# Kernel tuning notes

Measured on AMD Instinct MI355X. Metric: run time of the kernel, lower is better.

Reference implementation:

```python
import jax, jax.numpy as jnp
import numpy as np
import math

D_MODEL = 1024
NUM_HEADS = 16
D_K = D_MODEL // NUM_HEADS
MAX_LEN = 512
B, S = 16, 512


def setup_inputs() -> dict:
    key = jax.random.key(0)
    ks = jax.random.split(key, 12)
    init = lambda k, shape, s=0.02: jax.random.normal(k, shape, dtype=jnp.float32) * s
    return {
        "query": jax.random.normal(ks[0], (B, S, D_MODEL), dtype=jnp.float32),
        "key": jax.random.normal(ks[1], (B, S, D_MODEL), dtype=jnp.float32),
        "value": jax.random.normal(ks[2], (B, S, D_MODEL), dtype=jnp.float32),
        "wq_w": init(ks[3], (D_MODEL, D_MODEL)),
        "wq_b": jnp.zeros((D_MODEL,), jnp.float32),
        "wk_w": init(ks[4], (D_MODEL, D_MODEL)),
        "wk_b": jnp.zeros((D_MODEL,), jnp.float32),
        "wv_w": init(ks[5], (D_MODEL, D_MODEL)),
        "wv_b": jnp.zeros((D_MODEL,), jnp.float32),
        "wo_w": init(ks[6], (D_MODEL, D_MODEL)),
        "wo_b": jnp.zeros((D_MODEL,), jnp.float32),
        "rel_bias": init(ks[7], (NUM_HEADS, MAX_LEN, MAX_LEN)),
    }


def reference(query, key, value, wq_w, wq_b, wk_w, wk_b, wv_w, wv_b, wo_w, wo_b, rel_bias):
    b, s, _ = query.shape
    scale = math.sqrt(D_K)
    # torch Linear: x @ W.T + b ; split heads -> [b, s, H, dk]
    Q = (query @ wq_w.T + wq_b).reshape(b, s, NUM_HEADS, D_K)
    K = (key @ wk_w.T + wk_b).reshape(b, s, NUM_HEADS, D_K)
    V = (value @ wv_w.T + wv_b).reshape(b, s, NUM_HEADS, D_K)
    # scores [b, H, s, t]
    scores = jnp.einsum("bshd,bthd->bhst", Q, K) / scale
    scores = scores + rel_bias[None, :, :s, :s]
    causal = jnp.triu(jnp.ones((s, s), dtype=bool), k=1)  # True above diagonal
    scores = jnp.where(causal[None, None, :, :], -jnp.inf, scores)
    attn = jax.nn.softmax(scores, axis=-1)  # dropout p=0 (eval)
    ctx = jnp.einsum("bhst,bthd->bshd", attn, V).reshape(b, s, D_MODEL)
    out = ctx @ wo_w.T + wo_b
    return out, attn.mean(axis=1)
```

## Files before the change

kernel.cpp:

```cpp
#include <hip/hip_runtime.h>
#include <hip/hip_bf16.h>
#include <math.h>

#define D_MODEL 1024
#define NUM_HEADS 16
#define D_K 64
#define BATCH 16
#define SEQ 512

typedef __attribute__((ext_vector_type(8))) short short8;
typedef __attribute__((ext_vector_type(4))) float floatx4;

__device__ inline unsigned short f2bf(float f) {
  __hip_bfloat16 h = __float2bfloat16(f);
  return *reinterpret_cast<unsigned short*>(&h);
}
__device__ inline float bf2f(unsigned short us) {
  unsigned u = ((unsigned)us) << 16;
  return __uint_as_float(u);
}

typedef const __attribute__((address_space(1))) unsigned int glb_u32;
typedef __attribute__((address_space(3))) unsigned int lds_u32;

__device__ inline void load16_to_lds(const void* g, void* l) {
  __builtin_amdgcn_global_load_lds((glb_u32*)(uintptr_t)g,
                                   (lds_u32*)(unsigned int)(uintptr_t)l, 16, 0,
                                   0);
}

__global__ __launch_bounds__(256) void conv_all(
    const float* __restrict__ q, const float* __restrict__ k,
    const float* __restrict__ v, const float* __restrict__ w0,
    const float* __restrict__ w1, const float* __restrict__ w2,
    const float* __restrict__ w3, unsigned short* __restrict__ xq,
    unsigned short* __restrict__ xk, unsigned short* __restrict__ xv,
    unsigned short* __restrict__ d0, unsigned short* __restrict__ d1,
    unsigned short* __restrict__ d2, unsigned short* __restrict__ d3) {
  const size_t MG = 1048576, WG = 131072;
  const size_t g = (size_t)blockIdx.x * 256 + threadIdx.x;
  const float* src;
  unsigned short* dst;
  size_t idx;
  if (g < 3 * MG) {
    const int r = (int)(g >> 20);
    idx = g & (MG - 1);
    src = (r == 0) ? q : (r == 1) ? k : v;
    dst = (r == 0) ? xq : (r == 1) ? xk : xv;
  } else {
    const size_t gw = g - 3 * MG;
    const int r = (int)(gw >> 17);
    idx = gw & (WG - 1);
    src = (r == 0) ? w0 : (r == 1) ? w1 : (r == 2) ? w2 : w3;
    dst = (r == 0) ? d0 : (r == 1) ? d1 : (r == 2) ? d2 : d3;
  }
  const float4 a = ((const float4*)src)[2 * idx];
  const float4 b = ((const float4*)src)[2 * idx + 1];
  short8 o;
  o[0] = f2bf(a.x); o[1] = f2bf(a.y); o[2] = f2bf(a.z); o[3] = f2bf(a.w);
  o[4] = f2bf(b.x); o[5] = f2bf(b.y); o[6] = f2bf(b.z); o[7] = f2bf(b.w);
  ((short8*)dst)[idx] = o;
}

__global__ __launch_bounds__(256) void qkv_gemm(
    const unsigned short* __restrict__ Xall,
    const unsigned short* __restrict__ Wall,
    const float* __restrict__ bq, const float* __restrict__ bk,
    const float* __restrict__ bv,
    unsigned short* __restrict__ QKout,
    unsigned short* __restrict__ Vt) {
  constexpr int K = 1024;
  const size_t ME = (size_t)BATCH * SEQ * D_MODEL;
  const size_t WE = (size_t)D_MODEL * D_MODEL;

  const int f = blockIdx.x + (blockIdx.y << 3) + (blockIdx.z << 9);
  const int virt = ((f & 7) * 192) + (f >> 3);
  const int xi = virt & 7;
  const int rest = virt >> 3;
  const int yi = rest & 63;
  const int z = rest >> 6;

  const unsigned short* A = Xall + (size_t)z * ME;
  const unsigned short* Bw = Wall + (size_t)z * WE;
  const float* bias = (z == 0) ? bq : (z == 1) ? bk : bv;

  __shared__ __align__(16) unsigned short sA[2][128 * 64];
  __shared__ __align__(16) unsigned short sB[2][128 * 64];
  const int tid = threadIdx.x;
  const int w = tid >> 6, lane = tid & 63;
  const int quad = lane >> 4, lq = lane & 15;
  const int wm = w >> 1, wn = w & 1;
  const int m0 = yi << 7, n0 = xi << 7;

  const int lrow8 = lane >> 3;
  const int sg = lane & 7;

  floatx4 acc[4][4];
#pragma unroll
  for (int i = 0; i < 4; ++i)
#pragma unroll
    for (int j = 0; j < 4; ++j) acc[i][j] = {0.f, 0.f, 0.f, 0.f};

  auto stage = [&](int buf, int kt) {
#pragma unroll
    for (int i = 0; i < 4; ++i) {
      const int row = (i << 5) + (w << 3) + lrow8;
      const int g = sg ^ (row & 7);
      const unsigned short* gA = A + (size_t)(m0 + row) * K + kt + (g << 3);
      const unsigned short* gB = Bw + (size_t)(n0 + row) * K + kt + (g << 3);
      load16_to_lds(gA, &sA[buf][((i << 5) + (w << 3)) * 64]);
      load16_to_lds(gB, &sB[buf][((i << 5) + (w << 3)) * 64]);
    }
  };

  stage(0, 0);
  __syncthreads();
  int cur = 0;
  for (int kt = 0; kt < K; kt += 64) {
    if (kt + 64 < K) stage(cur ^ 1, kt + 64);
#pragma unroll
    for (int s = 0; s < 2; ++s) {
      short8 aF[4], bF[4];
#pragma unroll
      for (int mi = 0; mi < 4; ++mi) {
        const int row = (wm << 6) + (mi << 4) + lq;
        const int g = ((s << 2) + quad) ^ (row & 7);
        aF[mi] = *(const short8*)&sA[cur][row * 64 + (g << 3)];
      }
#pragma unroll
      for (int ni = 0; ni < 4; ++ni) {
        const int row = (wn << 6) + (ni << 4) + lq;
        const int g = ((s << 2) + quad) ^ (row & 7);
        bF[ni] = *(const short8*)&sB[cur][row * 64 + (g << 3)];
      }
#pragma unroll
      for (int mi = 0; mi < 4; ++mi)
#pragma unroll
        for (int ni = 0; ni < 4; ++ni)
          acc[mi][ni] = __builtin_amdgcn_mfma_f32_16x16x32_bf16(
              aF[mi], bF[ni], acc[mi][ni], 0, 0, 0);
    }
    __syncthreads();
    cur ^= 1;
  }

#pragma unroll
  for (int ni = 0; ni < 4; ++ni) {
    const int n = n0 + (wn << 6) + (ni << 4) + lq;
    const float bn = bias[n];
    const int hh = n >> 6, dk = n & 63;
#pragma unroll
    for (int mi = 0; mi < 4; ++mi) {
      const int mb = m0 + (wm << 6) + (mi << 4) + (quad << 2);
      const int bb = mb >> 9, ss = mb & 511;
      if (z == 2) {
        ushort4 pk;
        pk.x = f2bf(acc[mi][ni][0] + bn);
        pk.y = f2bf(acc[mi][ni][1] + bn);
        pk.z = f2bf(acc[mi][ni][2] + bn);
        pk.w = f2bf(acc[mi][ni][3] + bn);
        *(ushort4*)&Vt[((size_t)(bb * NUM_HEADS + hh) * D_K + dk) * SEQ + ss] =
            pk;
      } else {
        unsigned short* dst = QKout + (size_t)z * ME;
#pragma unroll
        for (int r = 0; r < 4; ++r)
          dst[((size_t)(bb * NUM_HEADS + hh) * SEQ + ss + r) * D_K + dk] =
              f2bf(acc[mi][ni][r] + bn);
      }
    }
  }
}

__global__ __launch_bounds__(256) void out_gemm(
    const unsigned short* __restrict__ A, const unsigned short* __restrict__ Bw,
    const float* __restrict__ bias, float* __restrict__ Cout) {
  constexpr int K = 1024;
  __shared__ __align__(16) unsigned short sA[2][128 * 64];
  __shared__ __align__(16) unsigned short sB[2][128 * 64];
  const int tid = threadIdx.x;
  const int w = tid >> 6, lane = tid & 63;
  const int quad = lane >> 4, lq = lane & 15;
  const int wm = w >> 1, wn = w & 1;

  const int f = blockIdx.x + (blockIdx.y << 3);
  const int virt = ((f & 7) << 6) + (f >> 3);
  const int m0 = (virt >> 3) << 7, n0 = (virt & 7) << 7;

  const int lrow8 = lane >> 3;
  const int sg = lane & 7;

  floatx4 acc[4][4];
#pragma unroll
  for (int i = 0; i < 4; ++i)
#pragma unroll
    for (int j = 0; j < 4; ++j) acc[i][j] = {0.f, 0.f, 0.f, 0.f};

  auto stage = [&](int buf, int kt) {
#pragma unroll
    for (int i = 0; i < 4; ++i) {
      const int row = (i << 5) + (w << 3) + lrow8;
      const int g = sg ^ (row & 7);
      const unsigned short* gA = A + (size_t)(m0 + row) * K + kt + (g << 3);
      const unsigned short* gB = Bw + (size_t)(n0 + row) * K + kt + (g << 3);
      load16_to_lds(gA, &sA[buf][((i << 5) + (w << 3)) * 64]);
      load16_to_lds(gB, &sB[buf][((i << 5) + (w << 3)) * 64]);
    }
  };

  stage(0, 0);
  __syncthreads();
  int cur = 0;
  for (int kt = 0; kt < K; kt += 64) {
    if (kt + 64 < K) stage(cur ^ 1, kt + 64);
#pragma unroll
    for (int s = 0; s < 2; ++s) {
      short8 aF[4], bF[4];
#pragma unroll
      for (int mi = 0; mi < 4; ++mi) {
        const int row = (wm << 6) + (mi << 4) + lq;
        const int g = ((s << 2) + quad) ^ (row & 7);
        aF[mi] = *(const short8*)&sA[cur][row * 64 + (g << 3)];
      }
#pragma unroll
      for (int ni = 0; ni < 4; ++ni) {
        const int row = (wn << 6) + (ni << 4) + lq;
        const int g = ((s << 2) + quad) ^ (row & 7);
        bF[ni] = *(const short8*)&sB[cur][row * 64 + (g << 3)];
      }
#pragma unroll
      for (int mi = 0; mi < 4; ++mi)
#pragma unroll
        for (int ni = 0; ni < 4; ++ni)
          acc[mi][ni] = __builtin_amdgcn_mfma_f32_16x16x32_bf16(
              aF[mi], bF[ni], acc[mi][ni], 0, 0, 0);
    }
    __syncthreads();
    cur ^= 1;
  }

#pragma unroll
  for (int ni = 0; ni < 4; ++ni) {
    const int n = n0 + (wn << 6) + (ni << 4) + lq;
    const float bn = bias[n];
#pragma unroll
    for (int mi = 0; mi < 4; ++mi) {
      const int mb = m0 + (wm << 6) + (mi << 4) + (quad << 2);
#pragma unroll
      for (int r = 0; r < 4; ++r)
        Cout[(size_t)(mb + r) * 1024 + n] = acc[mi][ni][r] + bn;
    }
  }
}

__global__ __launch_bounds__(512) void attn_mfma(
    const unsigned short* __restrict__ Qb,
    const unsigned short* __restrict__ Kb,
    const unsigned short* __restrict__ Vt,
    const float* __restrict__ rb,
    unsigned short* __restrict__ ctxb,
    unsigned short* __restrict__ Pg,
    float* __restrict__ flWS) {
  const int b = blockIdx.x;
  const int h = blockIdx.y;
  const int tid = threadIdx.x;
  const int w = tid >> 6, lane = tid & 63;
  const int quad = lane >> 4, lq = lane & 15;

  __shared__ __align__(16) unsigned short sK[512 * 64];
  __shared__ __align__(16) unsigned short sV[64 * 512];
  __shared__ __align__(16) unsigned short sPt[8][16][72];

  const size_t bh = (size_t)b * NUM_HEADS + h;
  const unsigned short* Qh = Qb + bh * SEQ * D_K;
  const unsigned short* Kh = Kb + bh * SEQ * D_K;
  const unsigned short* Vh = Vt + bh * D_K * SEQ;
  const float* rbh = rb + (size_t)h * SEQ * SEQ;

#pragma unroll
  for (int it = 0; it < 8; ++it) {
    const int L = (it << 13) + (tid << 4);
    {
      const int rk = L >> 7, ck = (L >> 4) & 7;
      load16_to_lds(
          (const unsigned char*)Kh + (L & ~127) + ((ck ^ (rk & 7)) << 4),
          (unsigned char*)sK + L);
    }
    {
      const int rv = L >> 10, cv = (L >> 4) & 63;
      load16_to_lds(
          (const unsigned char*)Vh + (L & ~1023) + ((cv ^ (rv & 7)) << 4),
          (unsigned char*)sV + L);
    }
  }
  __syncthreads();

#pragma unroll 1
  for (int si = 0; si < 4; ++si) {
    const int st = (si == 0) ? w : (si == 1) ? (15 - w)
                 : (si == 2) ? (16 + w) : (31 - w);
    const int qs = st << 4;
    const int nc = (st >> 2) + 1;

    short8 aQ0, aQ1;
    {
      const unsigned short* qrow = Qh + (size_t)(qs + lq) * D_K + (quad << 3);
      aQ0 = *(const short8*)(qrow);
      aQ1 = *(const short8*)(qrow + 32);
    }

    float lsum[4] = {0.f, 0.f, 0.f, 0.f};
    floatx4 O[4] = {{0.f, 0.f, 0.f, 0.f},
                    {0.f, 0.f, 0.f, 0.f},
                    {0.f, 0.f, 0.f, 0.f},
                    {0.f, 0.f, 0.f, 0.f}};

    const float* rbbase = rbh + (size_t)(qs + (quad << 2)) * SEQ + lq;
    float rbv[16];
#pragma unroll
    for (int nt = 0; nt < 4; ++nt)
#pragma unroll
      for (int r = 0; r < 4; ++r)
        rbv[nt * 4 + r] = rbbase[(size_t)r * SEQ + (nt << 4)];

    for (int c = 0; c < nc; ++c) {
      const int t0 = c << 6;
      float rbn[16];
      if (c + 1 < nc) {
        const float* rn = rbbase + t0 + 64;
#pragma unroll
        for (int nt = 0; nt < 4; ++nt)
#pragma unroll
          for (int r = 0; r < 4; ++r)
            rbn[nt * 4 + r] = rn[(size_t)r * SEQ + (nt << 4)];
      }

#pragma unroll
      for (int nt = 0; nt < 4; ++nt) {
        const int kr = t0 + (nt << 4) + lq;
        const unsigned char* kbase = (const unsigned char*)sK + (kr << 7);
        short8 bK0 = *(const short8*)(kbase + ((quad ^ (kr & 7)) << 4));
        short8 bK1 = *(const short8*)(kbase + (((quad + 4) ^ (kr & 7)) << 4));
        floatx4 s = {0.f, 0.f, 0.f, 0.f};
        s = __builtin_amdgcn_mfma_f32_16x16x32_bf16(aQ0, bK0, s, 0, 0, 0);
        s = __builtin_amdgcn_mfma_f32_16x16x32_bf16(aQ1, bK1, s, 0, 0, 0);
        const int col = t0 + (nt << 4) + lq;
#pragma unroll
        for (int r = 0; r < 4; ++r) {
          const int row = qs + (quad << 2) + r;
          float p = 0.f;
          if (col <= row) p = __expf(s[r] * 0.125f + rbv[nt * 4 + r]);
          lsum[r] += p;
          sPt[w][(quad << 2) + r][(nt << 4) + lq] = f2bf(p);
        }
      }

      short8 bV0[4], bV1[4];
#pragma unroll
      for (int nt = 0; nt < 4; ++nt) {
        const int vr = (nt << 4) + lq;
        const unsigned char* vbase = (const unsigned char*)sV + (vr << 10);
        const int cc = (t0 >> 3) + quad;
        bV0[nt] = *(const short8*)(vbase + ((cc ^ (vr & 7)) << 4));
        bV1[nt] = *(const short8*)(vbase + (((cc + 4) ^ (vr & 7)) << 4));
      }

      short8 aP0 = *(const short8*)&sPt[w][lq][quad << 3];
      short8 aP1 = *(const short8*)&sPt[w][lq][32 + (quad << 3)];

      {
        unsigned short* pgrow =
            Pg + (bh * SEQ + (qs + lq)) * SEQ + t0 + (quad << 3);
        *(short8*)pgrow = aP0;
        *(short8*)(pgrow + 32) = aP1;
      }

#pragma unroll
      for (int nt = 0; nt < 4; ++nt) {
        O[nt] = __builtin_amdgcn_mfma_f32_16x16x32_bf16(aP0, bV0[nt], O[nt], 0,
                                                        0, 0);
        O[nt] = __builtin_amdgcn_mfma_f32_16x16x32_bf16(aP1, bV1[nt], O[nt], 0,
                                                        0, 0);
      }

      if (c + 1 < nc) {
#pragma unroll
        for (int i = 0; i < 16; ++i) rbv[i] = rbn[i];
      }
    }

#pragma unroll
    for (int off = 1; off < 16; off <<= 1)
#pragma unroll
      for (int r = 0; r < 4; ++r) lsum[r] += __shfl_xor(lsum[r], off);
    float invl[4];
#pragma unroll
    for (int r = 0; r < 4; ++r) invl[r] = 1.f / lsum[r];
    if (lq == 0) {
#pragma unroll
      for (int r = 0; r < 4; ++r)
        flWS[bh * SEQ + qs + (quad << 2) + r] = invl[r] * 0.0625f;
    }
#pragma unroll
    for (int nt = 0; nt < 4; ++nt)
#pragma unroll
      for (int r = 0; r < 4; ++r) {
        const int row = qs + (quad << 2) + r;
        ctxb[((size_t)b * SEQ + row) * D_MODEL + h * D_K + (nt << 4) + lq] =
            f2bf(O[nt][r] * invl[r]);
      }
  }
}

__global__ __launch_bounds__(256) void attn_reduce(
    const unsigned short* __restrict__ Pg, const float* __restrict__ flWS,
    float* __restrict__ attn_mean) {
  const int b = blockIdx.x, rt = blockIdx.y, cs = blockIdx.z;
#pragma unroll
  for (int k = 0; k < 4; ++k) {
    const int slot = threadIdx.x + (k << 8);
    const int row = (rt << 6) + (slot >> 4);
    const int col0 = (cs << 7) + ((slot & 15) << 3);
    float acc[8] = {0.f, 0.f, 0.f, 0.f, 0.f, 0.f, 0.f, 0.f};
    if (col0 <= row) {
      for (int h = 0; h < NUM_HEADS; ++h) {
        const size_t base = (((size_t)b * NUM_HEADS + h) << 9) + row;
        const float f = flWS[base];
        const uint4 pk = *(const uint4*)&Pg[(base << 9) + col0];
        acc[0] += bf2f((unsigned short)(pk.x & 0xffff)) * f;
        acc[1] += bf2f((unsigned short)(pk.x >> 16)) * f;
        acc[2] += bf2f((unsigned short)(pk.y & 0xffff)) * f;
        acc[3] += bf2f((unsigned short)(pk.y >> 16)) * f;
        acc[4] += bf2f((unsigned short)(pk.z & 0xffff)) * f;
        acc[5] += bf2f((unsigned short)(pk.z >> 16)) * f;
        acc[6] += bf2f((unsigned short)(pk.w & 0xffff)) * f;
        acc[7] += bf2f((unsigned short)(pk.w >> 16)) * f;
      }
    }
    float4 o0, o1;
    o0.x = (col0 + 0 <= row) ? acc[0] : 0.f;
    o0.y = (col0 + 1 <= row) ? acc[1] : 0.f;
    o0.z = (col0 + 2 <= row) ? acc[2] : 0.f;
    o0.w = (col0 + 3 <= row) ? acc[3] : 0.f;
    o1.x = (col0 + 4 <= row) ? acc[4] : 0.f;
    o1.y = (col0 + 5 <= row) ? acc[5] : 0.f;
    o1.z = (col0 + 6 <= row) ? acc[6] : 0.f;
    o1.w = (col0 + 7 <= row) ? acc[7] : 0.f;
    float* dst = attn_mean + (((size_t)b << 9) + row) * SEQ + col0;
    *(float4*)dst = o0;
    *(float4*)(dst + 4) = o1;
  }
}

extern "C" void kernel_launch(void* const* d_in, const int* in_sizes, int n_in,
                              void* d_out, int out_size, void* d_ws,
                              size_t ws_size, hipStream_t stream) {
  const float* query = (const float*)d_in[0];
  const float* key_ = (const float*)d_in[1];
  const float* value = (const float*)d_in[2];
  const float* wq_w = (const float*)d_in[3];
  const float* wq_b = (const float*)d_in[4];
  const float* wk_w = (const float*)d_in[5];
  const float* wk_b = (const float*)d_in[6];
  const float* wv_w = (const float*)d_in[7];
  const float* wv_b = (const float*)d_in[8];
  const float* wo_w = (const float*)d_in[9];
  const float* wo_b = (const float*)d_in[10];
  const float* rel_bias = (const float*)d_in[11];

  float* out = (float*)d_out;
  float* attn_mean = out + (size_t)BATCH * SEQ * D_MODEL;

  const size_t ME = (size_t)BATCH * SEQ * D_MODEL;
  const size_t WE = (size_t)D_MODEL * D_MODEL;
  const size_t RE = (size_t)BATCH * NUM_HEADS * SEQ;

  unsigned short* Qb = (unsigned short*)d_ws;
  unsigned short* Kb = Qb + ME;
  unsigned short* Vt = Kb + ME;
  unsigned short* ctxb = Vt + ME;
  unsigned short* wob = ctxb + ME;
  float* flWS = (float*)(wob + WE);
  unsigned short* Pg = (unsigned short*)(flWS + RE);
  unsigned short* xq = Pg;
  unsigned short* xk = xq + ME;
  unsigned short* xv = xk + ME;
  unsigned short* wqb = xv + ME;
  unsigned short* wkb = wqb + WE;
  unsigned short* wvb = wkb + WE;

  conv_all<<<14336, 256, 0, stream>>>(query, key_, value, wq_w, wk_w, wv_w,
                                      wo_w, xq, xk, xv, wqb, wkb, wvb, wob);

  dim3 qkvg(8, 64, 3);
  qkv_gemm<<<qkvg, 256, 0, stream>>>(xq, wqb, wq_b, wk_b, wv_b, Qb, Vt);

  dim3 agrid(BATCH, NUM_HEADS);
  attn_mfma<<<agrid, 512, 0, stream>>>(Qb, Kb, Vt, rel_bias, ctxb, Pg, flWS);

  dim3 rgrid(BATCH, 8, 4);
  attn_reduce<<<rgrid, 256, 0, stream>>>(Pg, flWS, attn_mean);

  dim3 gblk(8, 64);
  out_gemm<<<gblk, 256, 0, stream>>>(ctxb, wob, wo_b, out);
}
```

Baseline: 316.6 us.

## Fuse fp32-to-bf16 activation conversion into QKV GEMM A-tile loading

Removes the separate pass that converts query/key/value to bf16. The QKV GEMM now loads fp32 activations into registers, converts them, and writes bf16 into LDS, with the global loads issued before the MFMA loop and the LDS writes after it. This avoids writing and re-reading a bf16 copy of the activations. In exchange, each GEMM block reads twice the bytes for A, reuses A across 8 column blocks from fp32, and uses more registers (launch bounds now request 2 blocks per SM).

```diff
diff --git a/kernel.cpp b/kernel.cpp
--- a/kernel.cpp
+++ b/kernel.cpp
@@ -29,31 +29,16 @@
                                    0);
 }
 
-__global__ __launch_bounds__(256) void conv_all(
-    const float* __restrict__ q, const float* __restrict__ k,
-    const float* __restrict__ v, const float* __restrict__ w0,
-    const float* __restrict__ w1, const float* __restrict__ w2,
-    const float* __restrict__ w3, unsigned short* __restrict__ xq,
-    unsigned short* __restrict__ xk, unsigned short* __restrict__ xv,
+__global__ __launch_bounds__(256) void conv_w(
+    const float* __restrict__ w0, const float* __restrict__ w1,
+    const float* __restrict__ w2, const float* __restrict__ w3,
     unsigned short* __restrict__ d0, unsigned short* __restrict__ d1,
     unsigned short* __restrict__ d2, unsigned short* __restrict__ d3) {
-  const size_t MG = 1048576, WG = 131072;
   const size_t g = (size_t)blockIdx.x * 256 + threadIdx.x;
-  const float* src;
-  unsigned short* dst;
-  size_t idx;
-  if (g < 3 * MG) {
-    const int r = (int)(g >> 20);
-    idx = g & (MG - 1);
-    src = (r == 0) ? q : (r == 1) ? k : v;
-    dst = (r == 0) ? xq : (r == 1) ? xk : xv;
-  } else {
-    const size_t gw = g - 3 * MG;
-    const int r = (int)(gw >> 17);
-    idx = gw & (WG - 1);
-    src = (r == 0) ? w0 : (r == 1) ? w1 : (r == 2) ? w2 : w3;
-    dst = (r == 0) ? d0 : (r == 1) ? d1 : (r == 2) ? d2 : d3;
-  }
+  const int r = (int)(g >> 17);
+  const size_t idx = g & 131071;
+  const float* src = (r == 0) ? w0 : (r == 1) ? w1 : (r == 2) ? w2 : w3;
+  unsigned short* dst = (r == 0) ? d0 : (r == 1) ? d1 : (r == 2) ? d2 : d3;
   const float4 a = ((const float4*)src)[2 * idx];
   const float4 b = ((const float4*)src)[2 * idx + 1];
   short8 o;
@@ -62,8 +47,9 @@
   ((short8*)dst)[idx] = o;
 }
 
-__global__ __launch_bounds__(256) void qkv_gemm(
-    const unsigned short* __restrict__ Xall,
+__global__ __launch_bounds__(256, 2) void qkv_gemm(
+    const float* __restrict__ Qf, const float* __restrict__ Kf,
+    const float* __restrict__ Vf,
     const unsigned short* __restrict__ Wall,
     const float* __restrict__ bq, const float* __restrict__ bk,
     const float* __restrict__ bv,
@@ -80,7 +66,7 @@
   const int yi = rest & 63;
   const int z = rest >> 6;
 
-  const unsigned short* A = Xall + (size_t)z * ME;
+  const float* A = (z == 0) ? Qf : (z == 1) ? Kf : Vf;
   const unsigned short* Bw = Wall + (size_t)z * WE;
   const float* bias = (z == 0) ? bq : (z == 1) ? bk : bv;
 
@@ -101,23 +87,51 @@
 #pragma unroll
     for (int j = 0; j < 4; ++j) acc[i][j] = {0.f, 0.f, 0.f, 0.f};
 
-  auto stage = [&](int buf, int kt) {
+  float4 a0[4], a1[4];
+
+  auto issueA = [&](int kt) {
 #pragma unroll
     for (int i = 0; i < 4; ++i) {
       const int row = (i << 5) + (w << 3) + lrow8;
       const int g = sg ^ (row & 7);
-      const unsigned short* gA = A + (size_t)(m0 + row) * K + kt + (g << 3);
+      const float* p = A + (size_t)(m0 + row) * K + kt + (g << 3);
+      a0[i] = *(const float4*)p;
+      a1[i] = *(const float4*)(p + 4);
+    }
+  };
+  auto writeA = [&](int buf) {
+#pragma unroll
+    for (int i = 0; i < 4; ++i) {
+      const int row = (i << 5) + (w << 3) + lrow8;
+      short8 o;
+      o[0] = f2bf(a0[i].x); o[1] = f2bf(a0[i].y);
+      o[2] = f2bf(a0[i].z); o[3] = f2bf(a0[i].w);
+      o[4] = f2bf(a1[i].x); o[5] = f2bf(a1[i].y);
+      o[6] = f2bf(a1[i].z); o[7] = f2bf(a1[i].w);
+      *(short8*)&sA[buf][row * 64 + (sg << 3)] = o;
+    }
+  };
+  auto stageB = [&](int buf, int kt) {
+#pragma unroll
+    for (int i = 0; i < 4; ++i) {
+      const int row = (i << 5) + (w << 3) + lrow8;
+      const int g = sg ^ (row & 7);
       const unsigned short* gB = Bw + (size_t)(n0 + row) * K + kt + (g << 3);
-      load16_to_lds(gA, &sA[buf][((i << 5) + (w << 3)) * 64]);
       load16_to_lds(gB, &sB[buf][((i << 5) + (w << 3)) * 64]);
     }
   };
 
-  stage(0, 0);
+  issueA(0);
+  stageB(0, 0);
+  writeA(0);
   __syncthreads();
+
   int cur = 0;
   for (int kt = 0; kt < K; kt += 64) {
-    if (kt + 64 < K) stage(cur ^ 1, kt + 64);
+    if (kt + 64 < K) {
+      issueA(kt + 64);
+      stageB(cur ^ 1, kt + 64);
+    }
 #pragma unroll
     for (int s = 0; s < 2; ++s) {
       short8 aF[4], bF[4];
@@ -140,6 +154,7 @@
           acc[mi][ni] = __builtin_amdgcn_mfma_f32_16x16x32_bf16(
               aF[mi], bF[ni], acc[mi][ni], 0, 0, 0);
     }
+    if (kt + 64 < K) writeA(cur ^ 1);
     __syncthreads();
     cur ^= 1;
   }
@@ -482,18 +497,15 @@
   unsigned short* wob = ctxb + ME;
   float* flWS = (float*)(wob + WE);
   unsigned short* Pg = (unsigned short*)(flWS + RE);
-  unsigned short* xq = Pg;
-  unsigned short* xk = xq + ME;
-  unsigned short* xv = xk + ME;
-  unsigned short* wqb = xv + ME;
+  unsigned short* wqb = Pg;
   unsigned short* wkb = wqb + WE;
   unsigned short* wvb = wkb + WE;
 
-  conv_all<<<14336, 256, 0, stream>>>(query, key_, value, wq_w, wk_w, wv_w,
-                                      wo_w, xq, xk, xv, wqb, wkb, wvb, wob);
+  conv_w<<<2048, 256, 0, stream>>>(wq_w, wk_w, wv_w, wo_w, wqb, wkb, wvb, wob);
 
   dim3 qkvg(8, 64, 3);
-  qkv_gemm<<<qkvg, 256, 0, stream>>>(xq, wqb, wq_b, wk_b, wv_b, Qb, Vt);
+  qkv_gemm<<<qkvg, 256, 0, stream>>>(query, key_, value, wqb, wq_b, wk_b,
+                                     wv_b, Qb, Vt);
 
   dim3 agrid(BATCH, NUM_HEADS);
   attn_mfma<<<agrid, 512, 0, stream>>>(Qb, Kb, Vt, rel_bias, ctxb, Pg, flWS);
```

After: 338.3 us. +6.9%, slower.

## Load QKV GEMM B fragments directly from global, skip causal mask off-diagonal

Applied to the files above, without the earlier changes.

The QKV GEMM stops staging weight tiles in LDS and has each lane read its B fragments straight from global memory, halving shared memory use and raising the occupancy hint to 4 blocks per CU. The attention kernel applies the causal comparison only on the diagonal chunk and computes exp unconditionally on earlier chunks. The global B loads are not coalesced and are reused only across waves through cache, so load latency may be exposed inside the MFMA loop.

```diff
diff --git a/kernel.cpp b/kernel.cpp
--- a/kernel.cpp
+++ b/kernel.cpp
@@ -62,7 +62,7 @@
   ((short8*)dst)[idx] = o;
 }
 
-__global__ __launch_bounds__(256) void qkv_gemm(
+__global__ __launch_bounds__(256, 4) void qkv_gemm(
     const unsigned short* __restrict__ Xall,
     const unsigned short* __restrict__ Wall,
     const float* __restrict__ bq, const float* __restrict__ bk,
@@ -85,7 +85,6 @@
   const float* bias = (z == 0) ? bq : (z == 1) ? bk : bv;
 
   __shared__ __align__(16) unsigned short sA[2][128 * 64];
-  __shared__ __align__(16) unsigned short sB[2][128 * 64];
   const int tid = threadIdx.x;
   const int w = tid >> 6, lane = tid & 63;
   const int quad = lane >> 4, lq = lane & 15;
@@ -101,37 +100,37 @@
 #pragma unroll
     for (int j = 0; j < 4; ++j) acc[i][j] = {0.f, 0.f, 0.f, 0.f};
 
-  auto stage = [&](int buf, int kt) {
+  const unsigned short* browp[4];
+#pragma unroll
+  for (int ni = 0; ni < 4; ++ni)
+    browp[ni] = Bw + (size_t)(n0 + (wn << 6) + (ni << 4) + lq) * K;
+
+  auto stageA = [&](int buf, int kt) {
 #pragma unroll
     for (int i = 0; i < 4; ++i) {
       const int row = (i << 5) + (w << 3) + lrow8;
       const int g = sg ^ (row & 7);
       const unsigned short* gA = A + (size_t)(m0 + row) * K + kt + (g << 3);
-      const unsigned short* gB = Bw + (size_t)(n0 + row) * K + kt + (g << 3);
       load16_to_lds(gA, &sA[buf][((i << 5) + (w << 3)) * 64]);
-      load16_to_lds(gB, &sB[buf][((i << 5) + (w << 3)) * 64]);
     }
   };
 
-  stage(0, 0);
+  stageA(0, 0);
   __syncthreads();
   int cur = 0;
   for (int kt = 0; kt < K; kt += 64) {
-    if (kt + 64 < K) stage(cur ^ 1, kt + 64);
+    if (kt + 64 < K) stageA(cur ^ 1, kt + 64);
 #pragma unroll
     for (int s = 0; s < 2; ++s) {
       short8 aF[4], bF[4];
+#pragma unroll
+      for (int ni = 0; ni < 4; ++ni)
+        bF[ni] = *(const short8*)(browp[ni] + kt + (s << 5) + (quad << 3));
 #pragma unroll
       for (int mi = 0; mi < 4; ++mi) {
         const int row = (wm << 6) + (mi << 4) + lq;
         const int g = ((s << 2) + quad) ^ (row & 7);
         aF[mi] = *(const short8*)&sA[cur][row * 64 + (g << 3)];
-      }
-#pragma unroll
-      for (int ni = 0; ni < 4; ++ni) {
-        const int row = (wn << 6) + (ni << 4) + lq;
-        const int g = ((s << 2) + quad) ^ (row & 7);
-        bF[ni] = *(const short8*)&sB[cur][row * 64 + (g << 3)];
       }
 #pragma unroll
       for (int mi = 0; mi < 4; ++mi)
@@ -325,6 +324,7 @@
 
     for (int c = 0; c < nc; ++c) {
       const int t0 = c << 6;
+      const bool diag = (c == nc - 1);
       float rbn[16];
       if (c + 1 < nc) {
         const float* rn = rbbase + t0 + 64;
@@ -344,14 +344,23 @@
         floatx4 s = {0.f, 0.f, 0.f, 0.f};
         s = __builtin_amdgcn_mfma_f32_16x16x32_bf16(aQ0, bK0, s, 0, 0, 0);
         s = __builtin_amdgcn_mfma_f32_16x16x32_bf16(aQ1, bK1, s, 0, 0, 0);
-        const int col = t0 + (nt << 4) + lq;
-#pragma unroll
-        for (int r = 0; r < 4; ++r) {
-          const int row = qs + (quad << 2) + r;
-          float p = 0.f;
-          if (col <= row) p = __expf(s[r] * 0.125f + rbv[nt * 4 + r]);
-          lsum[r] += p;
-          sPt[w][(quad << 2) + r][(nt << 4) + lq] = f2bf(p);
+        if (diag) {
+          const int col = t0 + (nt << 4) + lq;
+#pragma unroll
+          for (int r = 0; r < 4; ++r) {
+            const int row = qs + (quad << 2) + r;
+            float p = 0.f;
+            if (col <= row) p = __expf(s[r] * 0.125f + rbv[nt * 4 + r]);
+            lsum[r] += p;
+            sPt[w][(quad << 2) + r][(nt << 4) + lq] = f2bf(p);
+          }
+        } else {
+#pragma unroll
+          for (int r = 0; r < 4; ++r) {
+            const float p = __expf(s[r] * 0.125f + rbv[nt * 4 + r]);
+            lsum[r] += p;
+            sPt[w][(quad << 2) + r][(nt << 4) + lq] = f2bf(p);
+          }
         }
       }
 
```

After: 362.7 us. 14.5% more time.
